# Optimization experiments

Measured on AMD Instinct MI355X. Metric: run time of the kernel, lower is better.

## Reference

```python
import jax, jax.numpy as jnp
import numpy as np

PH, PW = 7, 7
SPATIAL_SCALE = 1.0


def setup_inputs() -> dict:
    key = jax.random.key(0)
    kf, kb, kx, ky = jax.random.split(key, 4)
    B, C, H, W, R = 4, 256, 50, 50, 300
    feature_maps = jax.random.normal(kf, (B, C, H, W), dtype=jnp.float32)
    bidx = jax.random.randint(kb, (R,), 0, B).astype(jnp.float32)
    xs = jax.random.uniform(kx, (R, 2), minval=0.0, maxval=W - 1.0)
    ys = jax.random.uniform(ky, (R, 2), minval=0.0, maxval=H - 1.0)
    x_min = jnp.min(xs, axis=1)
    x_max = jnp.max(xs, axis=1)
    y_min = jnp.min(ys, axis=1)
    y_max = jnp.max(ys, axis=1)
    rois = jnp.stack([x_min, y_min, x_max, y_max, bidx], axis=1)  # [R,5]
    return {"feature_maps": feature_maps, "rois": rois}


def _roi_pool(feature_maps, rois):
    B, C, H, W = feature_maps.shape
    s = SPATIAL_SCALE
    r = rois * s                              # first scale application (as in source)
    batch_idx = r[:, 4].astype(jnp.int32)     # int() truncation of scaled batch index
    # second scale application + round + clamp, faithful to source's double-scaling
    x0 = jnp.clip(jnp.round(r[:, 0] * s), 0, W - 1).astype(jnp.int32)
    x1 = jnp.clip(jnp.round(r[:, 2] * s), 0, W - 1).astype(jnp.int32)
    y0 = jnp.clip(jnp.round(r[:, 1] * s), 0, H - 1).astype(jnp.int32)
    y1 = jnp.clip(jnp.round(r[:, 3] * s), 0, H - 1).astype(jnp.int32)
    x1 = jnp.maximum(x1, x0 + 1)
    y1 = jnp.maximum(y1, y0 + 1)
    roi_w = x1 - x0                           # >= 1, so every adaptive bin is nonempty
    roi_h = y1 - y0

    Kw = -(-W // PW)                          # max adaptive bin width  (ceil(W/PW))
    Kh = -(-H // PH)                          # max adaptive bin height (ceil(H/PH))

    # adaptive_max_pool2d bin edges: start = floor(i*size/out), end = ceil((i+1)*size/out)
    pw = jnp.arange(PW)
    wstart = x0[:, None] + (pw[None, :] * roi_w[:, None]) // PW                       # [R,PW]
    wend = x0[:, None] + ((pw[None, :] + 1) * roi_w[:, None] + PW - 1) // PW          # [R,PW]
    kw = jnp.arange(Kw)
    wpos = wstart[:, :, None] + kw[None, None, :]                                      # [R,PW,Kw]
    widx = jnp.clip(wpos, 0, W - 1)
    wvalid = wpos < wend[:, :, None]

    ph = jnp.arange(PH)
    hstart = y0[:, None] + (ph[None, :] * roi_h[:, None]) // PH
    hend = y0[:, None] + ((ph[None, :] + 1) * roi_h[:, None] + PH - 1) // PH
    kh = jnp.arange(Kh)
    hpos = hstart[:, :, None] + kh[None, None, :]                                      # [R,PH,Kh]
    hidx = jnp.clip(hpos, 0, H - 1)
    hvalid = hpos < hend[:, :, None]

    NEG = jnp.finfo(feature_maps.dtype).min
    fm = feature_maps[batch_idx]              # [R,C,H,W] per-ROI source map

    def gather_w(fm_r, widx_r):               # fm_r [C,H,W], widx_r [PW,Kw]
        return fm_r[:, :, widx_r]             # [C,H,PW,Kw]

    g = jax.vmap(gather_w)(fm, widx)          # [R,C,H,PW,Kw]
    A = jnp.max(jnp.where(wvalid[:, None, None, :, :], g, NEG), axis=-1)  # [R,C,H,PW]

    def gather_h(A_r, hidx_r):                # A_r [C,H,PW], hidx_r [PH,Kh]
        return A_r[:, hidx_r, :]              # [C,PH,Kh,PW]

    g2 = jax.vmap(gather_h)(A, hidx)          # [R,C,PH,Kh,PW]
    out = jnp.max(jnp.where(hvalid[:, None, :, :, None], g2, NEG), axis=3)  # [R,C,PH,PW]
    return out


def reference(feature_maps, rois):
    return _roi_pool(feature_maps, rois)
```

## Files before the change

### kernel.cpp

```cpp
#include <hip/hip_runtime.h>
#include <hip/hip_bf16.h>
#include <float.h>

#define B_  4
#define C_  256
#define H_  50
#define W_  50
#define R_  300
#define PH_ 7
#define PW_ 7
#define S_  (H_ * W_)
#define Q_  (PH_ * PW_)
#define SC_ (S_ * C_)
#define CQ_  64
#define NCQ  (C_ / CQ_)
#define NWG_POOL (R_ * NCQ)

__global__ __launch_bounds__(256) void transpose_tables(
    const float* __restrict__ fm,
    float* __restrict__ fmT,
    float* __restrict__ P2,
    float* __restrict__ P4)
{
    __shared__ float tile[64][69];

    const int b  = blockIdx.z;
    const int c0 = blockIdx.y * 64;
    const int s0 = blockIdx.x * 64;

    const int tx = threadIdx.x;
    const int ty = threadIdx.y;

    if (s0 + tx < S_) {
        #pragma unroll
        for (int j = 0; j < 16; ++j) {
            const int c = c0 + ty + j * 4;
            tile[ty + j * 4][tx] = fm[((size_t)b * C_ + c) * S_ + (s0 + tx)];
        }
    }
    if (tx < 4 && s0 + 64 + tx < S_) {
        #pragma unroll
        for (int j = 0; j < 16; ++j) {
            const int c = c0 + ty + j * 4;
            tile[ty + j * 4][64 + tx] = fm[((size_t)b * C_ + c) * S_ + (s0 + 64 + tx)];
        }
    }
    __syncthreads();

    #pragma unroll
    for (int j = 0; j < 16; ++j) {
        const int s = s0 + ty + j * 4;
        if (s < S_) {
            const int ls  = ty + j * 4;
            const int w   = s % W_;
            const int rem = W_ - 1 - w;
            const float v0 = tile[tx][ls];
            float p2 = (rem >= 1) ? fmaxf(v0, tile[tx][ls + 1]) : v0;
            float p4 = p2;
            if (rem >= 2) p4 = fmaxf(p4, tile[tx][ls + 2]);
            if (rem >= 3) p4 = fmaxf(p4, tile[tx][ls + 3]);

            const size_t o = ((size_t)b * S_ + s) * C_ + (c0 + tx);
            fmT[o] = v0;
            P2[o]  = p2;
            P4[o]  = p4;
        }
    }
}

__device__ __forceinline__ void roi_decode(const float* __restrict__ rois, int r,
                                           int& b, int& x0, int& y0,
                                           int& roi_w, int& roi_h)
{
    const float* rp = rois + r * 5;
    b = (int)rp[4];
    x0      = (int)rintf(rp[0]);
    y0      = (int)rintf(rp[1]);
    int x1  = (int)rintf(rp[2]);
    int y1  = (int)rintf(rp[3]);
    x0 = min(max(x0, 0), W_ - 1);
    x1 = min(max(x1, 0), W_ - 1);
    y0 = min(max(y0, 0), H_ - 1);
    y1 = min(max(y1, 0), H_ - 1);
    x1 = max(x1, x0 + 1);
    y1 = max(y1, y0 + 1);
    roi_w = x1 - x0;
    roi_h = y1 - y0;
}

template<int WH>
__device__ __forceinline__ void pool_bins(
    const float* __restrict__ fmT, const float* __restrict__ P2,
    const float* __restrict__ P4, float* __restrict__ buf,
    int wv, int lane, size_t imgC,
    int x0, int y0, int roi_w, int roi_h)
{
    const int start = wv * 12 + (wv ? 1 : 0);
    const int qlast = wv * 12 + 12;

    #pragma unroll
    for (int k = 0; k < 13; ++k) {
        int q = start + k;
        q = (q > qlast) ? qlast : q;
        const int ph = q / PW_;
        const int pw = q - ph * PW_;
        const int ws = x0 + (pw * roi_w) / PW_;
        const int we = x0 + ((pw + 1) * roi_w + PW_ - 1) / PW_;
        const int hs = y0 + (ph * roi_h) / PH_;
        const int he = y0 + ((ph + 1) * roi_h + PH_ - 1) / PH_;
        const int ww = we - ws;

        const int sp = (ww >= 4) ? 4 : ((ww >= 2) ? 2 : 1);
        const float* tb = (ww >= 4) ? P4 : ((ww >= 2) ? P2 : fmT);
        const int colB = we - sp;

        float va[WH], vb[WH];
        #pragma unroll
        for (int kh = 0; kh < WH; ++kh) {
            int row = hs + kh;
            row = (row > he - 1) ? (he - 1) : row;
            const size_t ro = imgC + (size_t)(row * W_) * C_;
            va[kh] = tb[ro + (size_t)ws * C_];
            vb[kh] = tb[ro + (size_t)colB * C_];
        }
        float m = -FLT_MAX;
        #pragma unroll
        for (int kh = 0; kh < WH; ++kh)
            m = fmaxf(m, fmaxf(va[kh], vb[kh]));

        buf[q * 65 + lane] = m;
    }
}

__global__ __launch_bounds__(256) void roi_pool_tables(
    const float* __restrict__ fmT,
    const float* __restrict__ P2,
    const float* __restrict__ P4,
    const float* __restrict__ rois,
    float* __restrict__ out)
{
    __shared__ float buf[Q_ * 65];

    const int bid = blockIdx.x;
    const int swz = (bid & 7) * (NWG_POOL / 8) + (bid >> 3);
    const int r   = swz >> 2;
    const int c0  = (swz & (NCQ - 1)) * CQ_;

    const int t    = threadIdx.x;
    const int wv   = t >> 6;
    const int lane = t & 63;

    int b, x0, y0, roi_w, roi_h;
    roi_decode(rois, r, b, x0, y0, roi_w, roi_h);

    int whmax = 1;
    #pragma unroll
    for (int i = 0; i < PH_; ++i) {
        const int hs = (i * roi_h) / PH_;
        const int he = ((i + 1) * roi_h + PH_ - 1) / PH_;
        whmax = max(whmax, he - hs);
    }

    const size_t imgC = (size_t)b * SC_ + (size_t)(c0 + lane);

    switch (whmax) {
        case 1: pool_bins<1>(fmT, P2, P4, buf, wv, lane, imgC, x0, y0, roi_w, roi_h); break;
        case 2: pool_bins<2>(fmT, P2, P4, buf, wv, lane, imgC, x0, y0, roi_w, roi_h); break;
        case 3: pool_bins<3>(fmT, P2, P4, buf, wv, lane, imgC, x0, y0, roi_w, roi_h); break;
        case 4: pool_bins<4>(fmT, P2, P4, buf, wv, lane, imgC, x0, y0, roi_w, roi_h); break;
        case 5: pool_bins<5>(fmT, P2, P4, buf, wv, lane, imgC, x0, y0, roi_w, roi_h); break;
        case 6: pool_bins<6>(fmT, P2, P4, buf, wv, lane, imgC, x0, y0, roi_w, roi_h); break;
        case 7: pool_bins<7>(fmT, P2, P4, buf, wv, lane, imgC, x0, y0, roi_w, roi_h); break;
        default: pool_bins<8>(fmT, P2, P4, buf, wv, lane, imgC, x0, y0, roi_w, roi_h); break;
    }
    __syncthreads();

    float* outp = out + ((size_t)r * C_ + c0) * Q_;
    #pragma unroll
    for (int k = 0; k < 13; ++k) {
        const int e = k * 256 + t;
        if (e < CQ_ * Q_) {
            const int cl = e / Q_;
            const int q  = e - cl * Q_;
            outp[e] = buf[q * 65 + cl];
        }
    }
}

__global__ __launch_bounds__(256) void roi_pool_naive(
    const float* __restrict__ fm,
    const float* __restrict__ rois,
    float* __restrict__ out)
{
    const int total = R_ * C_ * Q_;
    int t = blockIdx.x * blockDim.x + threadIdx.x;
    if (t >= total) return;
    int q   = t % Q_;
    int tmp = t / Q_;
    int pw  = q % PW_;
    int ph  = q / PW_;
    int c   = tmp % C_;
    int r   = tmp / C_;

    int b, x0, y0, roi_w, roi_h;
    roi_decode(rois, r, b, x0, y0, roi_w, roi_h);

    const int ws = x0 + (pw * roi_w) / PW_;
    const int we = x0 + ((pw + 1) * roi_w + PW_ - 1) / PW_;
    const int hs = y0 + (ph * roi_h) / PH_;
    const int he = y0 + ((ph + 1) * roi_h + PH_ - 1) / PH_;

    const float* p = fm + ((size_t)(b * C_ + c)) * S_;
    float m = -FLT_MAX;
    for (int h = hs; h < he; ++h)
        for (int w = ws; w < we; ++w)
            m = fmaxf(m, p[h * W_ + w]);
    out[t] = m;
}

extern "C" void kernel_launch(void* const* d_in, const int* in_sizes, int n_in,
                              void* d_out, int out_size, void* d_ws, size_t ws_size,
                              hipStream_t stream)
{
    const float* fm   = (const float*)d_in[0];
    const float* rois = (const float*)d_in[1];
    float* out        = (float*)d_out;

    const size_t ARR  = (size_t)B_ * SC_;
    const size_t NEED = 3 * ARR * sizeof(float);

    if (ws_size >= NEED) {
        float* fmT = (float*)d_ws;
        float* P2  = fmT + ARR;
        float* P4  = P2 + ARR;
        {
            dim3 grid((S_ + 63) / 64, C_ / 64, B_);
            dim3 block(64, 4, 1);
            transpose_tables<<<grid, block, 0, stream>>>(fm, fmT, P2, P4);
        }
        roi_pool_tables<<<NWG_POOL, 256, 0, stream>>>(fmT, P2, P4, rois, out);
    } else {
        const int total = R_ * C_ * Q_;
        roi_pool_naive<<<(total + 255) / 256, 256, 0, stream>>>(fm, rois, out);
    }
}
```

Before: 33.72 us.

## Pool two channels per lane with float2 loads and 512-thread blocks

```diff
diff --git a/kernel.cpp b/kernel.cpp
--- a/kernel.cpp
+++ b/kernel.cpp
@@ -12,9 +12,8 @@
 #define S_  (H_ * W_)
 #define Q_  (PH_ * PW_)
 #define SC_ (S_ * C_)
-#define CQ_  64
-#define NCQ  (C_ / CQ_)
-#define NWG_POOL (R_ * NCQ)
+#define C2_ 128
+#define NWG2 (R_ * 2)
 
 __global__ __launch_bounds__(256) void transpose_tables(
     const float* __restrict__ fm,
@@ -89,62 +88,61 @@
 }
 
 template<int WH>
-__device__ __forceinline__ void pool_bins(
-    const float* __restrict__ fmT, const float* __restrict__ P2,
-    const float* __restrict__ P4, float* __restrict__ buf,
-    int wv, int lane, size_t imgC,
+__device__ __forceinline__ void pool_bins2(
+    const float2* __restrict__ t1, const float2* __restrict__ t2,
+    const float2* __restrict__ t4, float2* __restrict__ buf2,
+    int wv, int lane, size_t laneOff,
     int x0, int y0, int roi_w, int roi_h)
 {
-    const int start = wv * 12 + (wv ? 1 : 0);
-    const int qlast = wv * 12 + 12;
-
-    #pragma unroll
-    for (int k = 0; k < 13; ++k) {
-        int q = start + k;
-        q = (q > qlast) ? qlast : q;
-        const int ph = q / PW_;
-        const int pw = q - ph * PW_;
-        const int ws = x0 + (pw * roi_w) / PW_;
-        const int we = x0 + ((pw + 1) * roi_w + PW_ - 1) / PW_;
-        const int hs = y0 + (ph * roi_h) / PH_;
-        const int he = y0 + ((ph + 1) * roi_h + PH_ - 1) / PH_;
-        const int ww = we - ws;
-
-        const int sp = (ww >= 4) ? 4 : ((ww >= 2) ? 2 : 1);
-        const float* tb = (ww >= 4) ? P4 : ((ww >= 2) ? P2 : fmT);
-        const int colB = we - sp;
-
-        float va[WH], vb[WH];
-        #pragma unroll
-        for (int kh = 0; kh < WH; ++kh) {
-            int row = hs + kh;
-            row = (row > he - 1) ? (he - 1) : row;
-            const size_t ro = imgC + (size_t)(row * W_) * C_;
-            va[kh] = tb[ro + (size_t)ws * C_];
-            vb[kh] = tb[ro + (size_t)colB * C_];
-        }
-        float m = -FLT_MAX;
-        #pragma unroll
-        for (int kh = 0; kh < WH; ++kh)
-            m = fmaxf(m, fmaxf(va[kh], vb[kh]));
-
-        buf[q * 65 + lane] = m;
-    }
-}
-
-__global__ __launch_bounds__(256) void roi_pool_tables(
+    #pragma unroll 2
+    for (int k = 0; k < 7; ++k) {
+        const int q = wv + 8 * k;
+        if (q < Q_) {
+            const int ph = q / PW_;
+            const int pw = q - ph * PW_;
+            const int ws = x0 + (pw * roi_w) / PW_;
+            const int we = x0 + ((pw + 1) * roi_w + PW_ - 1) / PW_;
+            const int hs = y0 + (ph * roi_h) / PH_;
+            const int he = y0 + ((ph + 1) * roi_h + PH_ - 1) / PH_;
+            const int ww = we - ws;
+
+            const int sp = (ww >= 4) ? 4 : ((ww >= 2) ? 2 : 1);
+            const float2* tb = (ww >= 4) ? t4 : ((ww >= 2) ? t2 : t1);
+            const int colB = we - sp;
+
+            float2 va[WH], vb[WH];
+            #pragma unroll
+            for (int kh = 0; kh < WH; ++kh) {
+                int row = hs + kh;
+                row = (row > he - 1) ? (he - 1) : row;
+                const size_t ro = laneOff + (size_t)(row * W_) * C2_;
+                va[kh] = tb[ro + (size_t)ws * C2_];
+                vb[kh] = tb[ro + (size_t)colB * C2_];
+            }
+            float mx = -FLT_MAX, my = -FLT_MAX;
+            #pragma unroll
+            for (int kh = 0; kh < WH; ++kh) {
+                mx = fmaxf(mx, fmaxf(va[kh].x, vb[kh].x));
+                my = fmaxf(my, fmaxf(va[kh].y, vb[kh].y));
+            }
+            buf2[q * 65 + lane] = make_float2(mx, my);
+        }
+    }
+}
+
+__global__ __launch_bounds__(512) void roi_pool_tables2(
     const float* __restrict__ fmT,
     const float* __restrict__ P2,
     const float* __restrict__ P4,
     const float* __restrict__ rois,
     float* __restrict__ out)
 {
-    __shared__ float buf[Q_ * 65];
+    __shared__ float2 buf2[Q_ * 65];
 
     const int bid = blockIdx.x;
-    const int swz = (bid & 7) * (NWG_POOL / 8) + (bid >> 3);
-    const int r   = swz >> 2;
-    const int c0  = (swz & (NCQ - 1)) * CQ_;
+    const int swz = (bid & 7) * (NWG2 / 8) + (bid >> 3);
+    const int r   = swz >> 1;
+    const int hh  = swz & 1;
 
     const int t    = threadIdx.x;
     const int wv   = t >> 6;
@@ -161,28 +159,32 @@
         whmax = max(whmax, he - hs);
     }
 
-    const size_t imgC = (size_t)b * SC_ + (size_t)(c0 + lane);
+    const size_t laneOff = (size_t)b * (S_ * C2_) + (size_t)(hh * 64 + lane);
+    const float2* t1 = (const float2*)fmT;
+    const float2* t2 = (const float2*)P2;
+    const float2* t4 = (const float2*)P4;
 
     switch (whmax) {
-        case 1: pool_bins<1>(fmT, P2, P4, buf, wv, lane, imgC, x0, y0, roi_w, roi_h); break;
-        case 2: pool_bins<2>(fmT, P2, P4, buf, wv, lane, imgC, x0, y0, roi_w, roi_h); break;
-        case 3: pool_bins<3>(fmT, P2, P4, buf, wv, lane, imgC, x0, y0, roi_w, roi_h); break;
-        case 4: pool_bins<4>(fmT, P2, P4, buf, wv, lane, imgC, x0, y0, roi_w, roi_h); break;
-        case 5: pool_bins<5>(fmT, P2, P4, buf, wv, lane, imgC, x0, y0, roi_w, roi_h); break;
-        case 6: pool_bins<6>(fmT, P2, P4, buf, wv, lane, imgC, x0, y0, roi_w, roi_h); break;
-        case 7: pool_bins<7>(fmT, P2, P4, buf, wv, lane, imgC, x0, y0, roi_w, roi_h); break;
-        default: pool_bins<8>(fmT, P2, P4, buf, wv, lane, imgC, x0, y0, roi_w, roi_h); break;
+        case 1: pool_bins2<1>(t1, t2, t4, buf2, wv, lane, laneOff, x0, y0, roi_w, roi_h); break;
+        case 2: pool_bins2<2>(t1, t2, t4, buf2, wv, lane, laneOff, x0, y0, roi_w, roi_h); break;
+        case 3: pool_bins2<3>(t1, t2, t4, buf2, wv, lane, laneOff, x0, y0, roi_w, roi_h); break;
+        case 4: pool_bins2<4>(t1, t2, t4, buf2, wv, lane, laneOff, x0, y0, roi_w, roi_h); break;
+        case 5: pool_bins2<5>(t1, t2, t4, buf2, wv, lane, laneOff, x0, y0, roi_w, roi_h); break;
+        case 6: pool_bins2<6>(t1, t2, t4, buf2, wv, lane, laneOff, x0, y0, roi_w, roi_h); break;
+        case 7: pool_bins2<7>(t1, t2, t4, buf2, wv, lane, laneOff, x0, y0, roi_w, roi_h); break;
+        default: pool_bins2<8>(t1, t2, t4, buf2, wv, lane, laneOff, x0, y0, roi_w, roi_h); break;
     }
     __syncthreads();
 
-    float* outp = out + ((size_t)r * C_ + c0) * Q_;
+    float* outp = out + ((size_t)r * C_ + hh * C2_) * Q_;
+    const float* bufs = (const float*)buf2;
     #pragma unroll
     for (int k = 0; k < 13; ++k) {
-        const int e = k * 256 + t;
-        if (e < CQ_ * Q_) {
+        const int e = k * 512 + t;
+        if (e < C2_ * Q_) {
             const int cl = e / Q_;
             const int q  = e - cl * Q_;
-            outp[e] = buf[q * 65 + cl];
+            outp[e] = bufs[(q * 65 + (cl >> 1)) * 2 + (cl & 1)];
         }
     }
 }
@@ -238,7 +240,7 @@
             dim3 block(64, 4, 1);
             transpose_tables<<<grid, block, 0, stream>>>(fm, fmT, P2, P4);
         }
-        roi_pool_tables<<<NWG_POOL, 256, 0, stream>>>(fmT, P2, P4, rois, out);
+        roi_pool_tables2<<<NWG2, 512, 0, stream>>>(fmT, P2, P4, rois, out);
     } else {
         const int total = R_ * C_ * Q_;
         roi_pool_naive<<<(total + 255) / 256, 256, 0, stream>>>(fm, rois, out);
```

New measurement: 35.66 us. 5.7% more time.
